# Performance work log

Hardware: AMD Instinct MI355X
Metric: run time of the kernel (lower is better)

## Reference

```python
import jax, jax.numpy as jnp
from jax import lax
import numpy as np

B, T, TW, EW = 32, 64, 32, 300   # dialogues, utterances, words, word-embed
H = 512                          # lstm hidden per direction
E = 2 * H                        # utterance embedding size
HH = 512                         # emotion hidden size
C = 7                            # output classes


def setup_inputs() -> dict:
    key = jax.random.key(0)
    ks = jax.random.split(key, 24)
    n = lambda k, shp: (jax.random.normal(k, shp, dtype=jnp.float32) * 0.05)
    inp = {
        "input_data": jax.random.normal(ks[0], (B, T, TW, EW), dtype=jnp.float32),
        # BiLSTM (torch gate order i,f,g,o)
        "lstm_Wih_f": n(ks[1], (4 * H, EW)), "lstm_Whh_f": n(ks[2], (4 * H, H)), "lstm_b_f": n(ks[3], (4 * H,)),
        "lstm_Wih_b": n(ks[4], (4 * H, EW)), "lstm_Whh_b": n(ks[5], (4 * H, H)), "lstm_b_b": n(ks[6], (4 * H,)),
        # attention weight
        "W_att": n(ks[7], (E, E)),
        # global-state GRUCell (torch gate order r,z,n)
        "g_Wih": n(ks[8], (3 * E, E)), "g_Whh": n(ks[9], (3 * E, E)), "g_bih": n(ks[10], (3 * E,)), "g_bhh": n(ks[11], (3 * E,)),
        # party-state GRUCell
        "p_Wih": n(ks[12], (3 * E, E)), "p_Whh": n(ks[13], (3 * E, E)), "p_bih": n(ks[14], (3 * E,)), "p_bhh": n(ks[15], (3 * E,)),
        # emotion-state GRUCell (input E, hidden HH)
        "e_Wih": n(ks[16], (3 * HH, E)), "e_Whh": n(ks[17], (3 * HH, HH)), "e_bih": n(ks[18], (3 * HH,)), "e_bhh": n(ks[19], (3 * HH,)),
        # classifier
        "cls_W": n(ks[20], (C, HH)), "cls_b": n(ks[21], (C,)),
    }
    return inp


def _gru_cell(x, h, Wih, Whh, bih, bhh):
    gi = x @ Wih.T + bih
    gh = h @ Whh.T + bhh
    ir, iz, inn = jnp.split(gi, 3, axis=-1)
    hr, hz, hn = jnp.split(gh, 3, axis=-1)
    r = jax.nn.sigmoid(ir + hr)
    z = jax.nn.sigmoid(iz + hz)
    n = jnp.tanh(inn + r * hn)
    return (1.0 - z) * n + z * h


def _lstm_last_hidden(xs, Wih, Whh, b):
    # xs: [Tw, N, Ew] -> final hidden [N, H]
    N = xs.shape[1]
    h0 = jnp.zeros((N, H), xs.dtype)

    def step(carry, x):
        h, c = carry
        g = x @ Wih.T + h @ Whh.T + b
        i_, f_, g_, o_ = jnp.split(g, 4, axis=-1)
        c2 = jax.nn.sigmoid(f_) * c + jax.nn.sigmoid(i_) * jnp.tanh(g_)
        h2 = jax.nn.sigmoid(o_) * jnp.tanh(c2)
        return (h2, c2), None

    (h, _), _ = lax.scan(step, (h0, h0), xs)
    return h


def _forward(input_data, lstm_Wih_f, lstm_Whh_f, lstm_b_f, lstm_Wih_b, lstm_Whh_b, lstm_b_b,
             W_att, g_Wih, g_Whh, g_bih, g_bhh, p_Wih, p_Whh, p_bih, p_bhh,
             e_Wih, e_Whh, e_bih, e_bhh, cls_W, cls_b):
    # ---- FeatureExtraction: BiLSTM over words, take fwd-last + bwd-first hidden ----
    x = input_data.reshape(B * T, TW, EW).transpose(1, 0, 2)          # [Tw, N, Ew]
    h_fwd = _lstm_last_hidden(x, lstm_Wih_f, lstm_Whh_f, lstm_b_f)     # [N, H]
    h_bwd = _lstm_last_hidden(x[::-1], lstm_Wih_b, lstm_Whh_b, lstm_b_b)  # [N, H]
    feats = jnp.concatenate([h_fwd, h_bwd], axis=-1).reshape(B, T, E)  # [B, T, 2H]

    # ---- EmotionDetection: sequential recurrence over utterances ----
    utt = feats.transpose(1, 0, 2)                                     # [T, B, E]
    hist0 = jnp.zeros((T + 1, B, E), feats.dtype)   # global_state history (idx 0 = zero init)
    party0 = jnp.zeros((2, B, E), feats.dtype)
    emo0 = jnp.zeros((B, HH), feats.dtype)
    l_idx = jnp.arange(T + 1)[:, None]              # [T+1, 1]

    def step(carry, inp):
        hist, party, emo = carry
        x_i, i = inp
        p = i % 2
        g_prev = hist[i]                                               # global_state[i]
        new_g = _gru_cell(x_i + party[p], g_prev, g_Wih, g_Whh, g_bih, g_bhh)
        hist = hist.at[i + 1].set(new_g)
        # attention over history indices 0..i (excludes the just-appended state)
        q = x_i @ W_att                                                # [B, E]
        scores = jnp.einsum('be,lbe->lb', q, hist)                     # [T+1, B]
        scores = jnp.where(l_idx <= i, scores, -jnp.inf)
        w = jax.nn.softmax(scores, axis=0)[:, :, None]                 # [T+1, B, 1]
        context = jnp.sum(hist * w, axis=0)                            # [B, E]
        new_p = _gru_cell(x_i + context, party[p], p_Wih, p_Whh, p_bih, p_bhh)
        party = party.at[p].set(new_p)
        emo = _gru_cell(new_p, emo, e_Wih, e_Whh, e_bih, e_bhh)        # [B, HH]
        return (hist, party, emo), emo

    _, emo_seq = lax.scan(step, (hist0, party0, emo0), (utt, jnp.arange(T)))
    emo_seq = emo_seq.transpose(1, 0, 2)                               # [B, T, HH]
    return emo_seq @ cls_W.T + cls_b                                   # [B, T, C]


def reference(input_data, lstm_Wih_f, lstm_Whh_f, lstm_b_f, lstm_Wih_b, lstm_Whh_b, lstm_b_b,
              W_att, g_Wih, g_Whh, g_bih, g_bhh, p_Wih, p_Whh, p_bih, p_bhh,
              e_Wih, e_Whh, e_bih, e_bhh, cls_W, cls_b):
    return _forward(input_data, lstm_Wih_f, lstm_Whh_f, lstm_b_f, lstm_Wih_b, lstm_Whh_b, lstm_b_b,
                    W_att, g_Wih, g_Whh, g_bih, g_bhh, p_Wih, p_Whh, p_bih, p_bhh,
                    e_Wih, e_Whh, e_bih, e_bhh, cls_W, cls_b)
```

## Files before the change

kernel.cpp:

```cpp
#include <hip/hip_runtime.h>
#include <math.h>

#define B_  32
#define T_  64
#define TW_ 32
#define EW_ 300
#define H_  512
#define E_  1024
#define HH_ 512
#define C_  7
#define N_  2048

typedef float f32x4 __attribute__((ext_vector_type(4)));
typedef short s16x8 __attribute__((ext_vector_type(8)));
typedef unsigned short u16;
typedef unsigned int u32;

__device__ __forceinline__ float sigm(float x){ return 1.f/(1.f+expf(-x)); }
__device__ __forceinline__ float bf2f(u16 u){
  union{float f; unsigned v;} x; x.v = ((unsigned)u)<<16; return x.f;
}
__device__ __forceinline__ u16 f2bf(float f){
  union{float f; unsigned v;} x; x.f = f;
  unsigned r = x.v + 0x7FFF + ((x.v>>16)&1);
  return (u16)(r>>16);
}
__device__ __forceinline__ void g2lds16(const void* g, void* l){
  __builtin_amdgcn_global_load_lds((const __attribute__((address_space(1))) u32*)g,
                                   (__attribute__((address_space(3))) u32*)l, 16, 0, 0);
}

__global__ __launch_bounds__(256) void k_pack_w(
    const float* __restrict__ Wih_f, const float* __restrict__ Whh_f,
    const float* __restrict__ Wih_b, const float* __restrict__ Whh_b,
    u16* __restrict__ Wpk)
{
  size_t idx = (size_t)blockIdx.x*256 + threadIdx.x;
  if(idx >= (size_t)32*26*4096) return;
  int c   = (int)(idx & 31);
  int row = (int)((idx >> 5) & 127);
  int kc  = (int)((idx >> 12) % 26);
  int pan = (int)(idx / ((size_t)26*4096));
  int dir = pan >> 4, mt = pan & 15;
  int g = row >> 5, ml = row & 31;
  int R = g*512 + mt*32 + ml;
  int k = kc*32 + c;
  const float* Wih = dir ? Wih_b : Wih_f;
  const float* Whh = dir ? Whh_b : Whh_f;
  float v = (k < 320) ? ((k < EW_) ? Wih[(size_t)R*EW_ + k] : 0.f)
                      : Whh[(size_t)R*H_ + (k-320)];
  Wpk[idx] = f2bf(v);
}

__global__ __launch_bounds__(256) void k_pack_x(
    const float* __restrict__ input, u16* __restrict__ xpk)
{
  size_t idx = (size_t)blockIdx.x*256 + threadIdx.x;
  if(idx >= (size_t)32*16*10*4096) return;
  int c   = (int)(idx & 31);
  int row = (int)((idx >> 5) & 127);
  int kc  = (int)((idx >> 12) % 10);
  int q2  = (int)((idx >> 12) / 10);
  int nt  = q2 & 15, wt = q2 >> 4;
  int n = nt*128 + row;
  int k = kc*32 + c;
  float v = (k < EW_) ? input[((size_t)n*TW_ + wt)*EW_ + k] : 0.f;
  xpk[idx] = f2bf(v);
}

__global__ __launch_bounds__(256) void k_f2bf(const float* __restrict__ src,
                                              u16* __restrict__ dst, int n)
{
  int idx = blockIdx.x*256 + threadIdx.x;
  if(idx < n) dst[idx] = f2bf(src[idx]);
}

__global__ __launch_bounds__(256) void k_wattT(const float* __restrict__ W,
                                               u16* __restrict__ dst)
{
  int idx = blockIdx.x*256 + threadIdx.x;
  if(idx >= E_*E_) return;
  int j = idx >> 10, k = idx & 1023;
  dst[idx] = f2bf(W[(size_t)k*E_ + j]);
}

__global__ __launch_bounds__(256) void lstm3(
    const u16* __restrict__ xpk, const u16* __restrict__ Wpk,
    const float* __restrict__ b_f, const float* __restrict__ b_b,
    const u16* __restrict__ hpk_in, u16* __restrict__ hpk_out,
    float* __restrict__ cb, u16* __restrict__ featsbf, int t)
{
  const int panel = blockIdx.x, nt = blockIdx.y;
  const int dir = panel & 1, mt = panel >> 1;
  const int wt = dir ? (TW_-1-t) : t;
  const u16* srcW = Wpk + (size_t)(dir*16+mt)*26*4096;
  const u16* srcX = xpk + (size_t)(wt*16+nt)*10*4096;
  const u16* srcH = hpk_in + (size_t)(dir*16+nt)*16*4096;

  __shared__ __align__(16) u16 As[3][4096];
  __shared__ __align__(16) u16 Bs[3][4096];

  const int tid = threadIdx.x;
  const int w = tid >> 6, l = tid & 63;
  const int lr = l & 15, lh = l >> 4;
  const int wn = w >> 1, wm = w & 1;

  f32x4 acc[4][4];
  #pragma unroll
  for(int a=0;a<4;a++)
    #pragma unroll
    for(int g=0;g<4;g++) acc[a][g] = (f32x4){0.f,0.f,0.f,0.f};

  auto stage = [&](int kc, int b){
    const u16* aB = (kc < 10) ? (srcX + (size_t)kc*4096) : (srcH + (size_t)(kc-10)*4096);
    const u16* bB = srcW + (size_t)kc*4096;
    #pragma unroll
    for(int c=0;c<2;++c){
      const int cc = w*2 + c;
      g2lds16((const char*)aB + cc*1024 + l*16, (char*)&As[b][0] + cc*1024);
      g2lds16((const char*)bB + cc*1024 + l*16, (char*)&Bs[b][0] + cc*1024);
    }
  };

  stage(0, 0);
  stage(1, 1);
  #pragma unroll
  for(int kc=0; kc<26; ++kc){
    if(kc < 25) asm volatile("s_waitcnt vmcnt(4)" ::: "memory");
    else        asm volatile("s_waitcnt vmcnt(0)" ::: "memory");
    __builtin_amdgcn_s_barrier();
    __builtin_amdgcn_sched_barrier(0);
    if(kc+2 < 26) stage(kc+2, (kc+2)%3);
    const int cu = kc % 3;
    s16x8 av[4], bv[4];
    #pragma unroll
    for(int nf=0; nf<4; ++nf)
      av[nf] = *(const s16x8*)&As[cu][(wn*64 + nf*16 + lr)*32 + lh*8];
    #pragma unroll
    for(int g=0; g<4; ++g)
      bv[g] = *(const s16x8*)&Bs[cu][(g*32 + wm*16 + lr)*32 + lh*8];
    #pragma unroll
    for(int g=0; g<4; ++g)
      #pragma unroll
      for(int nf=0; nf<4; ++nf)
        acc[nf][g] = __builtin_amdgcn_mfma_f32_16x16x32_bf16(av[nf], bv[g], acc[nf][g], 0,0,0);
  }

  const float* bias = dir ? b_b : b_f;
  const int col = wm*16 + lr;
  const int m = mt*32 + col;
  const float bi = bias[m], bfv = bias[H_+m], bg = bias[2*H_+m], bo = bias[3*H_+m];
  float* cbp = cb + (size_t)dir*N_*H_;
  u16* hop = hpk_out + ((size_t)(dir*16+nt)*16 + mt)*4096;
  const int n0 = nt*128;
  #pragma unroll
  for(int nf=0; nf<4; ++nf){
    #pragma unroll
    for(int r=0; r<4; ++r){
      const int row = wn*64 + nf*16 + lh*4 + r;
      const int n = n0 + row;
      float gi = acc[nf][0][r] + bi;
      float gf = acc[nf][1][r] + bfv;
      float gc = acc[nf][2][r] + bg;
      float go = acc[nf][3][r] + bo;
      float c_old = cbp[(size_t)n*H_ + m];
      float c2 = sigm(gf)*c_old + sigm(gi)*tanhf(gc);
      float h2 = sigm(go)*tanhf(c2);
      cbp[(size_t)n*H_ + m] = c2;
      if(t == TW_-1) featsbf[(size_t)n*E_ + dir*H_ + m] = f2bf(h2);
      else           hop[row*32 + col] = f2bf(h2);
    }
  }
}

__global__ __launch_bounds__(256) void k_qgemm(const u16* __restrict__ featsbf,
                                               const u16* __restrict__ WattT,
                                               float* __restrict__ q)
{
  const int n0 = blockIdx.x*64, j0 = blockIdx.y*64;
  __shared__ __align__(16) u16 As[64*40];
  __shared__ __align__(16) u16 Bs[64*40];
  const int tid = threadIdx.x;
  const int w = tid>>6, l = tid&63, lr = l&15, lk = (l>>4)*8;
  const int arow = tid>>2, ak8 = (tid&3)*8;

  f32x4 acc[4];
  #pragma unroll
  for(int i=0;i<4;i++) acc[i] = (f32x4){0.f,0.f,0.f,0.f};

  for(int kc=0; kc<32; ++kc){
    *(s16x8*)&As[arow*40 + ak8] = *(const s16x8*)&featsbf[(size_t)(n0+arow)*E_ + kc*32 + ak8];
    *(s16x8*)&Bs[arow*40 + ak8] = *(const s16x8*)&WattT[(size_t)(j0+arow)*E_ + kc*32 + ak8];
    __syncthreads();
    s16x8 av = *(const s16x8*)&As[(w*16 + lr)*40 + lk];
    #pragma unroll
    for(int mf=0; mf<4; ++mf){
      s16x8 bv = *(const s16x8*)&Bs[(mf*16 + lr)*40 + lk];
      acc[mf] = __builtin_amdgcn_mfma_f32_16x16x32_bf16(av, bv, acc[mf], 0,0,0);
    }
    __syncthreads();
  }
  #pragma unroll
  for(int mf=0; mf<4; ++mf)
    #pragma unroll
    for(int r=0; r<4; ++r){
      int n = n0 + w*16 + (l>>4)*4 + r;
      q[(size_t)n*E_ + j0 + mf*16 + lr] = acc[mf][r];
    }
}

struct GArg2 {
  const u16* xA; const u16* xB;
  long ldA; long ldB;
  const u16* W; int K;
};

__device__ __forceinline__ void gemm32v2(const GArg2 a, int R, int xt, int ks,
                                         int KS, int z, float* __restrict__ part,
                                         char* smem)
{
  u16* Xs0 = (u16*)smem;
  u16* Xs1 = Xs0 + 32*40;
  u16* Ws0 = Xs1 + 32*40;
  u16* Ws1 = Ws0 + 128*32;
  const int Kc = a.K / KS;
  const int nch = Kc >> 5;
  const int kb0 = ks * Kc;
  const int tid = threadIdx.x;
  const int w = tid>>6, l = tid&63, lr = l&15, lh = l>>4;

  f32x4 a00={0,0,0,0}, a01={0,0,0,0}, a10={0,0,0,0}, a11={0,0,0,0};

  auto issueW = [&](int c, u16* Wb){
    const int kb = kb0 + c*32;
    #pragma unroll
    for(int c2=0;c2<2;++c2){
      const int cc = w*2 + c2;
      const char* g = (const char*)(a.W + (size_t)(xt*128 + cc*16 + (l>>2))*a.K + kb) + (l&3)*16;
      g2lds16(g, (char*)Wb + cc*1024);
    }
  };
  auto loadX = [&](int c, short4* xr){
    const int kb = kb0 + c*32;
    const int row = tid>>3, k4 = (tid&7)*4;
    short4 xv = *(const short4*)&a.xA[(size_t)row*a.ldA + kb + k4];
    if(a.xB){
      short4 yv = *(const short4*)&a.xB[(size_t)row*a.ldB + kb + k4];
      xv.x = (short)f2bf(bf2f((u16)xv.x)+bf2f((u16)yv.x));
      xv.y = (short)f2bf(bf2f((u16)xv.y)+bf2f((u16)yv.y));
      xv.z = (short)f2bf(bf2f((u16)xv.z)+bf2f((u16)yv.z));
      xv.w = (short)f2bf(bf2f((u16)xv.w)+bf2f((u16)yv.w));
    }
    *xr = xv;
  };
  auto writeX = [&](short4 xv, u16* Xb){
    *(short4*)&Xb[(tid>>3)*40 + (tid&7)*4] = xv;
  };

  short4 xr;
  issueW(0, Ws0); loadX(0, &xr); writeX(xr, Xs0);
  __syncthreads();
  for(int c=0;c<nch;++c){
    u16* Xc = (c&1)?Xs1:Xs0; u16* Wc = (c&1)?Ws1:Ws0;
    u16* Xn = (c&1)?Xs0:Xs1; u16* Wn = (c&1)?Ws0:Ws1;
    const bool pre = (c+1 < nch);
    if(pre){ issueW(c+1, Wn); loadX(c+1, &xr); }
    s16x8 av0 = *(const s16x8*)&Xc[lr*40 + lh*8];
    s16x8 av1 = *(const s16x8*)&Xc[(16+lr)*40 + lh*8];
    s16x8 bv0 = *(const s16x8*)&Wc[(w*32 + lr)*32 + lh*8];
    s16x8 bv1 = *(const s16x8*)&Wc[(w*32 + 16 + lr)*32 + lh*8];
    a00 = __builtin_amdgcn_mfma_f32_16x16x32_bf16(av0, bv0, a00, 0,0,0);
    a01 = __builtin_amdgcn_mfma_f32_16x16x32_bf16(av0, bv1, a01, 0,0,0);
    a10 = __builtin_amdgcn_mfma_f32_16x16x32_bf16(av1, bv0, a10, 0,0,0);
    a11 = __builtin_amdgcn_mfma_f32_16x16x32_bf16(av1, bv1, a11, 0,0,0);
    if(pre) writeX(xr, Xn);
    __syncthreads();
  }
  float* dst = part + (size_t)((z*KS + ks)*B_)*R + xt*128 + w*32;
  f32x4 accs[2][2] = {{a00,a01},{a10,a11}};
  #pragma unroll
  for(int nf=0; nf<2; ++nf)
    #pragma unroll
    for(int mf=0; mf<2; ++mf)
      #pragma unroll
      for(int r=0; r<4; ++r){
        int n = nf*16 + lh*4 + r;
        dst[(size_t)n*R + mf*16 + lr] = accs[nf][mf][r];
      }
}

__device__ __forceinline__ void att_body(const float* __restrict__ q,
                                         const u16* __restrict__ histbf,
                                         const u16* __restrict__ featsbf,
                                         u16* __restrict__ xcbf,
                                         int i, int b, char* smem)
{
  float* qs = (float*)smem;
  float* sc = qs + E_;
  const int tid = threadIdx.x;
  *(float4*)&qs[tid*4] = *(const float4*)&q[((size_t)b*T_ + i)*E_ + tid*4];
  __syncthreads();
  const int wv = tid>>6, ln = tid&63;
  for(int L = wv; L <= i; L += 4){
    const u16* hl = histbf + ((size_t)L*B_ + b)*E_;
    float s = 0.f;
    s16x8 h0 = *(const s16x8*)&hl[ln*16];
    s16x8 h1 = *(const s16x8*)&hl[ln*16 + 8];
    #pragma unroll
    for(int j=0;j<8;j++){
      s += qs[ln*16 + j]     * bf2f((u16)h0[j]);
      s += qs[ln*16 + 8 + j] * bf2f((u16)h1[j]);
    }
    #pragma unroll
    for(int off=32; off; off>>=1) s += __shfl_down(s, off);
    if(ln == 0) sc[L] = s;
  }
  __syncthreads();
  if(tid < 64){
    float v  = (tid <= i) ? sc[tid] : -INFINITY;
    float mx = v;
    #pragma unroll
    for(int off=32; off; off>>=1) mx = fmaxf(mx, __shfl_xor(mx, off));
    float ex = (tid <= i) ? expf(v - mx) : 0.f;
    float sm = ex;
    #pragma unroll
    for(int off=32; off; off>>=1) sm += __shfl_xor(sm, off);
    sc[tid] = ex / sm;
  }
  __syncthreads();
  const int e4 = tid*4;
  float c0=0.f, c1=0.f, c2=0.f, c3=0.f;
  for(int L=0; L<=i; ++L){
    float wl = sc[L];
    short4 hv = *(const short4*)&histbf[((size_t)L*B_ + b)*E_ + e4];
    c0 += wl*bf2f((u16)hv.x);
    c1 += wl*bf2f((u16)hv.y);
    c2 += wl*bf2f((u16)hv.z);
    c3 += wl*bf2f((u16)hv.w);
  }
  const u16* xi = featsbf + ((size_t)b*T_ + i)*E_ + e4;
  xcbf[(size_t)b*E_ + e4 + 0] = f2bf(bf2f(xi[0]) + c0);
  xcbf[(size_t)b*E_ + e4 + 1] = f2bf(bf2f(xi[1]) + c1);
  xcbf[(size_t)b*E_ + e4 + 2] = f2bf(bf2f(xi[2]) + c2);
  xcbf[(size_t)b*E_ + e4 + 3] = f2bf(bf2f(xi[3]) + c3);
}

__device__ __forceinline__ void gru_comb(const float* __restrict__ part, int R, int J, int KS,
                                         const float* __restrict__ bih, const float* __restrict__ bhh,
                                         const float* __restrict__ hprev_f,
                                         float* __restrict__ dst_f,
                                         u16* __restrict__ dstbf,
                                         float* __restrict__ dst_seq, int idx)
{
  const int b = idx / J, e = idx - b*J;
  float ir=0.f, iz=0.f, in_=0.f, hr=0.f, hz=0.f, hn=0.f;
  for(int ks=0; ks<KS; ++ks){
    const float* p0 = part + (size_t)(ks*B_ + b)*R;
    const float* p1 = part + (size_t)((KS+ks)*B_ + b)*R;
    ir += p0[e]; iz += p0[J+e]; in_ += p0[2*J+e];
    hr += p1[e]; hz += p1[J+e]; hn  += p1[2*J+e];
  }
  ir += bih[e]; iz += bih[J+e]; in_ += bih[2*J+e];
  hr += bhh[e]; hz += bhh[J+e]; hn  += bhh[2*J+e];
  const float r = sigm(ir + hr);
  const float z = sigm(iz + hz);
  const float n = tanhf(in_ + r*hn);
  const float hp = hprev_f[(size_t)b*J + e];
  const float h2 = (1.f - z)*n + z*hp;
  dst_f[(size_t)b*J + e] = h2;
  dstbf[(size_t)b*J + e] = f2bf(h2);
  if(dst_seq) dst_seq[(size_t)b*J + e] = h2;
}

__global__ __launch_bounds__(256) void k_A(GArg2 g0, GArg2 g1, GArg2 e0, GArg2 e1,
    float* __restrict__ part_g, float* __restrict__ part_e,
    const float* __restrict__ q, const u16* __restrict__ histbf,
    const u16* __restrict__ featsbf, u16* __restrict__ xcbf, int i)
{
  __shared__ __align__(16) char smem[21504];
  const int x = blockIdx.x;
  if(x < 384){
    if(i >= T_) return;
    const int xt = x % 24, ks = (x/24) & 7, z = x/192;
    gemm32v2(z ? g1 : g0, 3*E_, xt, ks, 8, z, part_g, smem);
  } else if(x < 576){
    if(i < 1) return;
    const int ix = x-384, xt = ix % 12, ks = (ix/12) & 7, z = ix/96;
    gemm32v2(z ? e1 : e0, 3*HH_, xt, ks, 8, z, part_e, smem);
  } else {
    if(i >= T_) return;
    att_body(q, histbf, featsbf, xcbf, i, x-576, smem);
  }
}

__global__ __launch_bounds__(256) void k_B(GArg2 p0, GArg2 p1,
    const float* __restrict__ part_g, const float* __restrict__ part_e,
    const float* __restrict__ g_bih, const float* __restrict__ g_bhh,
    const float* __restrict__ e_bih, const float* __restrict__ e_bhh,
    const float* __restrict__ gf_prev, float* __restrict__ gf_next,
    u16* __restrict__ histbf,
    float* __restrict__ emof, u16* __restrict__ emobf,
    float* __restrict__ emo_seq, float* __restrict__ part_p, int i)
{
  __shared__ __align__(16) char smem[21504];
  const int x = blockIdx.x;
  if(x < 128){
    if(i >= T_) return;
    gru_comb(part_g, 3*E_, E_, 8, g_bih, g_bhh,
             gf_prev, gf_next, histbf + (size_t)(i+1)*B_*E_, nullptr,
             x*256 + (int)threadIdx.x);
  } else if(x < 512){
    if(i >= T_) return;
    const int ix = x-128, xt = ix % 24, ks = (ix/24) & 7, z = ix/192;
    gemm32v2(z ? p1 : p0, 3*E_, xt, ks, 8, z, part_p, smem);
  } else {
    if(i < 1) return;
    gru_comb(part_e, 3*HH_, HH_, 8, e_bih, e_bhh,
             emof, emof, emobf, emo_seq + (size_t)(i-1)*B_*HH_,
             (x-512)*256 + (int)threadIdx.x);
  }
}

__global__ __launch_bounds__(256) void k_C(const float* __restrict__ part_p,
    const float* __restrict__ p_bih, const float* __restrict__ p_bhh,
    float* __restrict__ partyf_p, u16* __restrict__ partybf_p)
{
  const int idx = blockIdx.x*256 + threadIdx.x;
  gru_comb(part_p, 3*E_, E_, 8, p_bih, p_bhh, partyf_p, partyf_p, partybf_p, nullptr, idx);
}

__global__ __launch_bounds__(256) void classify(const float* __restrict__ emo_seq,
    const float* __restrict__ clsW, const float* __restrict__ clsb, float* __restrict__ out)
{
  const int idx = blockIdx.x*256 + threadIdx.x;
  if(idx >= B_*T_*C_) return;
  const int c = idx % C_;
  const int bt = idx / C_;
  const int t = bt % T_, b = bt / T_;
  const float* e = emo_seq + (size_t)(t*B_ + b)*HH_;
  const float* w = clsW + (size_t)c*HH_;
  float s = clsb[c];
  for(int h=0; h<HH_; ++h) s += e[h]*w[h];
  out[idx] = s;
}

extern "C" void kernel_launch(void* const* d_in, const int* in_sizes, int n_in,
                              void* d_out, int out_size, void* d_ws, size_t ws_size,
                              hipStream_t stream)
{
  const float* input  = (const float*)d_in[0];
  const float* Wih_f  = (const float*)d_in[1];
  const float* Whh_f  = (const float*)d_in[2];
  const float* b_f    = (const float*)d_in[3];
  const float* Wih_b  = (const float*)d_in[4];
  const float* Whh_b  = (const float*)d_in[5];
  const float* b_b    = (const float*)d_in[6];
  const float* W_att  = (const float*)d_in[7];
  const float* g_Wih  = (const float*)d_in[8];
  const float* g_Whh  = (const float*)d_in[9];
  const float* g_bih  = (const float*)d_in[10];
  const float* g_bhh  = (const float*)d_in[11];
  const float* p_Wih  = (const float*)d_in[12];
  const float* p_Whh  = (const float*)d_in[13];
  const float* p_bih  = (const float*)d_in[14];
  const float* p_bhh  = (const float*)d_in[15];
  const float* e_Wih  = (const float*)d_in[16];
  const float* e_Whh  = (const float*)d_in[17];
  const float* e_bih  = (const float*)d_in[18];
  const float* e_bhh  = (const float*)d_in[19];
  const float* cls_W  = (const float*)d_in[20];
  const float* cls_b  = (const float*)d_in[21];

  char* base = (char*)d_ws;
  size_t off = 0;
  auto alloc = [&](size_t bytes)->char*{
    char* p = base + off; off += (bytes + 255) & ~(size_t)255; return p;
  };
  u16*   Wpk     = (u16*)alloc((size_t)32*26*4096*2);
  u16*   xpk     = (u16*)alloc((size_t)32*16*10*4096*2);
  u16*   hpkA    = (u16*)alloc((size_t)2*16*16*4096*2);
  u16*   hpkB    = (u16*)alloc((size_t)2*16*16*4096*2);
  float* cb      = (float*)alloc((size_t)2*N_*H_*4);
  u16*   featsbf = (u16*)alloc((size_t)N_*E_*2);
  u16*   eWih    = (u16*)alloc((size_t)3*HH_*E_*2);
  u16*   eWhh    = (u16*)alloc((size_t)3*HH_*HH_*2);
  u16*   histbf  = (u16*)alloc((size_t)(T_+1)*B_*E_*2);
  float* gfbuf   = (float*)alloc((size_t)2*B_*E_*4);
  float* partyf  = (float*)alloc((size_t)2*B_*E_*4);
  u16*   partybf = (u16*)alloc((size_t)2*B_*E_*2);
  float* emof    = (float*)alloc((size_t)B_*HH_*4);
  u16*   emobf   = (u16*)alloc((size_t)B_*HH_*2);
  float* emo_seq = (float*)alloc((size_t)T_*B_*HH_*4);
  u16*   xcbf    = (u16*)alloc((size_t)B_*E_*2);
  u16*   gWih    = (u16*)((char*)xpk + 0);
  u16*   gWhh    = (u16*)((char*)xpk + 6291456);
  u16*   pWih    = (u16*)((char*)xpk + 12582912);
  u16*   pWhh    = (u16*)((char*)xpk + 18874368);
  float* part_e  = (float*)((char*)xpk + 25165824);
  float* q       = (float*)((char*)xpk + 28311552);
  u16*   WattT   = (u16*)((char*)xpk + 36700160);
  float* part_g  = (float*)cb;
  float* part_p  = (float*)hpkA;

  hipMemsetAsync(hpkA,    0, (size_t)2*16*16*4096*2, stream);
  hipMemsetAsync(cb,      0, (size_t)2*N_*H_*4, stream);
  hipMemsetAsync(histbf,  0, (size_t)B_*E_*2, stream);
  hipMemsetAsync(gfbuf,   0, (size_t)B_*E_*4, stream);
  hipMemsetAsync(partyf,  0, (size_t)2*B_*E_*4, stream);
  hipMemsetAsync(partybf, 0, (size_t)2*B_*E_*2, stream);
  hipMemsetAsync(emof,    0, (size_t)B_*HH_*4, stream);
  hipMemsetAsync(emobf,   0, (size_t)B_*HH_*2, stream);

  k_pack_w<<<dim3(((size_t)32*26*4096 + 255)/256), 256, 0, stream>>>(Wih_f, Whh_f, Wih_b, Whh_b, Wpk);
  k_pack_x<<<dim3(((size_t)32*16*10*4096 + 255)/256), 256, 0, stream>>>(input, xpk);

  for(int t=0; t<TW_; ++t){
    u16* hin  = (t & 1) ? hpkB : hpkA;
    u16* hout = (t & 1) ? hpkA : hpkB;
    lstm3<<<dim3(32, 16), 256, 0, stream>>>(xpk, Wpk, b_f, b_b, hin, hout, cb, featsbf, t);
  }

  k_f2bf<<<dim3((3*E_*E_+255)/256), 256, 0, stream>>>(g_Wih, gWih, 3*E_*E_);
  k_f2bf<<<dim3((3*E_*E_+255)/256), 256, 0, stream>>>(g_Whh, gWhh, 3*E_*E_);
  k_f2bf<<<dim3((3*E_*E_+255)/256), 256, 0, stream>>>(p_Wih, pWih, 3*E_*E_);
  k_f2bf<<<dim3((3*E_*E_+255)/256), 256, 0, stream>>>(p_Whh, pWhh, 3*E_*E_);
  k_f2bf<<<dim3((3*HH_*E_+255)/256), 256, 0, stream>>>(e_Wih, eWih, 3*HH_*E_);
  k_f2bf<<<dim3((3*HH_*HH_+255)/256), 256, 0, stream>>>(e_Whh, eWhh, 3*HH_*HH_);
  k_wattT<<<dim3((E_*E_+255)/256), 256, 0, stream>>>(W_att, WattT);

  k_qgemm<<<dim3(32, 16), 256, 0, stream>>>(featsbf, WattT, q);

  for(int i=0; i<=T_; ++i){
    const int p  = i & 1;
    const int pe = (i-1) & 1;
    GArg2 ga0{ featsbf + (size_t)i*E_, partybf + (size_t)p*B_*E_, (long)T_*E_, (long)E_, gWih, E_ };
    GArg2 ga1{ histbf + (size_t)i*B_*E_, nullptr, (long)E_, 0, gWhh, E_ };
    GArg2 ea0{ partybf + (size_t)pe*B_*E_, nullptr, (long)E_, 0, eWih, E_ };
    GArg2 ea1{ emobf, nullptr, (long)HH_, 0, eWhh, HH_ };
    k_A<<<dim3(608), 256, 0, stream>>>(ga0, ga1, ea0, ea1, part_g, part_e,
                                       q, histbf, featsbf, xcbf, i);
    GArg2 pa0{ xcbf, nullptr, (long)E_, 0, pWih, E_ };
    GArg2 pa1{ partybf + (size_t)p*B_*E_, nullptr, (long)E_, 0, pWhh, E_ };
    k_B<<<dim3(576), 256, 0, stream>>>(pa0, pa1, part_g, part_e,
                                       g_bih, g_bhh, e_bih, e_bhh,
                                       gfbuf + (size_t)(i&1)*B_*E_,
                                       gfbuf + (size_t)((i+1)&1)*B_*E_,
                                       histbf, emof, emobf, emo_seq, part_p, i);
    if(i < T_){
      k_C<<<dim3(128), 256, 0, stream>>>(part_p, p_bih, p_bhh,
                                         partyf + (size_t)p*B_*E_,
                                         partybf + (size_t)p*B_*E_);
    }
  }

  classify<<<dim3((B_*T_*C_+255)/256), 256, 0, stream>>>(emo_seq, cls_W, cls_b, (float*)d_out);
}
```

Before: 2.666 ms.

## Fuse word-LSTM timesteps into one persistent kernel with group barriers

Replaces the 32 per-timestep LSTM launches with a single persistent kernel of 512 blocks that loops over time. The cell state now stays in registers instead of a global buffer, and each timestep synchronizes on per-group atomic counters, where a group is the 16 blocks sharing a direction and batch tile. The x-projection tiles for the next step are prefetched before the spin-wait. This removes launch overhead and the global cell-state traffic, but it requires all 512 blocks to be co-resident. With launch_bounds(256,2) that holds only if the device has enough CUs, otherwise the spin barrier can deadlock.

```diff
diff --git a/kernel.cpp b/kernel.cpp
--- a/kernel.cpp
+++ b/kernel.cpp
@@ -84,18 +84,16 @@
   dst[idx] = f2bf(W[(size_t)k*E_ + j]);
 }
 
-__global__ __launch_bounds__(256) void lstm3(
+__global__ __launch_bounds__(256, 2) void lstm_p(
     const u16* __restrict__ xpk, const u16* __restrict__ Wpk,
     const float* __restrict__ b_f, const float* __restrict__ b_b,
-    const u16* __restrict__ hpk_in, u16* __restrict__ hpk_out,
-    float* __restrict__ cb, u16* __restrict__ featsbf, int t)
-{
-  const int panel = blockIdx.x, nt = blockIdx.y;
-  const int dir = panel & 1, mt = panel >> 1;
-  const int wt = dir ? (TW_-1-t) : t;
+    u16* __restrict__ hpkA, u16* __restrict__ hpkB,
+    u16* __restrict__ featsbf, u32* __restrict__ bar)
+{
+  const int bx = blockIdx.x;
+  const int g  = bx & 31, mt = bx >> 5;
+  const int dir = g & 1, nt = g >> 1;
   const u16* srcW = Wpk + (size_t)(dir*16+mt)*26*4096;
-  const u16* srcX = xpk + (size_t)(wt*16+nt)*10*4096;
-  const u16* srcH = hpk_in + (size_t)(dir*16+nt)*16*4096;
 
   __shared__ __align__(16) u16 As[3][4096];
   __shared__ __align__(16) u16 Bs[3][4096];
@@ -105,14 +103,17 @@
   const int lr = l & 15, lh = l >> 4;
   const int wn = w >> 1, wm = w & 1;
 
-  f32x4 acc[4][4];
+  const float* bias = dir ? b_b : b_f;
+  const int col = wm*16 + lr;
+  const int m = mt*32 + col;
+  const float bi = bias[m], bfv = bias[H_+m], bg = bias[2*H_+m], bo = bias[3*H_+m];
+
+  float creg[4][4];
   #pragma unroll
-  for(int a=0;a<4;a++)
-    #pragma unroll
-    for(int g=0;g<4;g++) acc[a][g] = (f32x4){0.f,0.f,0.f,0.f};
-
-  auto stage = [&](int kc, int b){
-    const u16* aB = (kc < 10) ? (srcX + (size_t)kc*4096) : (srcH + (size_t)(kc-10)*4096);
+  for(int a=0;a<4;a++){ creg[a][0]=0.f; creg[a][1]=0.f; creg[a][2]=0.f; creg[a][3]=0.f; }
+
+  auto stage = [&](const u16* sX, const u16* sH, int kc, int b){
+    const u16* aB = (kc < 10) ? (sX + (size_t)kc*4096) : (sH + (size_t)(kc-10)*4096);
     const u16* bB = srcW + (size_t)kc*4096;
     #pragma unroll
     for(int c=0;c<2;++c){
@@ -122,53 +123,85 @@
     }
   };
 
-  stage(0, 0);
-  stage(1, 1);
-  #pragma unroll
-  for(int kc=0; kc<26; ++kc){
-    if(kc < 25) asm volatile("s_waitcnt vmcnt(4)" ::: "memory");
-    else        asm volatile("s_waitcnt vmcnt(0)" ::: "memory");
-    __builtin_amdgcn_s_barrier();
-    __builtin_amdgcn_sched_barrier(0);
-    if(kc+2 < 26) stage(kc+2, (kc+2)%3);
-    const int cu = kc % 3;
-    s16x8 av[4], bv[4];
-    #pragma unroll
-    for(int nf=0; nf<4; ++nf)
-      av[nf] = *(const s16x8*)&As[cu][(wn*64 + nf*16 + lr)*32 + lh*8];
-    #pragma unroll
-    for(int g=0; g<4; ++g)
-      bv[g] = *(const s16x8*)&Bs[cu][(g*32 + wm*16 + lr)*32 + lh*8];
-    #pragma unroll
-    for(int g=0; g<4; ++g)
+  {
+    const int wt0 = dir ? (TW_-1) : 0;
+    const u16* sX0 = xpk + (size_t)(wt0*16+nt)*10*4096;
+    stage(sX0, nullptr, 0, 0);
+    stage(sX0, nullptr, 1, 1);
+  }
+
+  #pragma unroll 1
+  for(int t=0; t<TW_; ++t){
+    const int wt = dir ? (TW_-1-t) : t;
+    const u16* sX = xpk + (size_t)(wt*16+nt)*10*4096;
+    const u16* hin  = (t & 1) ? hpkB : hpkA;
+    u16*       hout = (t & 1) ? hpkA : hpkB;
+    const u16* sH = hin + (size_t)(dir*16+nt)*16*4096;
+
+    f32x4 acc[4][4];
+    #pragma unroll
+    for(int a=0;a<4;a++)
+      #pragma unroll
+      for(int gg=0;gg<4;gg++) acc[a][gg] = (f32x4){0.f,0.f,0.f,0.f};
+
+    #pragma unroll
+    for(int kc=0; kc<26; ++kc){
+      if(kc < 25) asm volatile("s_waitcnt vmcnt(4)" ::: "memory");
+      else        asm volatile("s_waitcnt vmcnt(0)" ::: "memory");
+      __builtin_amdgcn_s_barrier();
+      __builtin_amdgcn_sched_barrier(0);
+      if(kc+2 < 26) stage(sX, sH, kc+2, (kc+2)%3);
+      const int cu = kc % 3;
+      s16x8 av[4], bv[4];
       #pragma unroll
       for(int nf=0; nf<4; ++nf)
-        acc[nf][g] = __builtin_amdgcn_mfma_f32_16x16x32_bf16(av[nf], bv[g], acc[nf][g], 0,0,0);
-  }
-
-  const float* bias = dir ? b_b : b_f;
-  const int col = wm*16 + lr;
-  const int m = mt*32 + col;
-  const float bi = bias[m], bfv = bias[H_+m], bg = bias[2*H_+m], bo = bias[3*H_+m];
-  float* cbp = cb + (size_t)dir*N_*H_;
-  u16* hop = hpk_out + ((size_t)(dir*16+nt)*16 + mt)*4096;
-  const int n0 = nt*128;
-  #pragma unroll
-  for(int nf=0; nf<4; ++nf){
-    #pragma unroll
-    for(int r=0; r<4; ++r){
-      const int row = wn*64 + nf*16 + lh*4 + r;
-      const int n = n0 + row;
-      float gi = acc[nf][0][r] + bi;
-      float gf = acc[nf][1][r] + bfv;
-      float gc = acc[nf][2][r] + bg;
-      float go = acc[nf][3][r] + bo;
-      float c_old = cbp[(size_t)n*H_ + m];
-      float c2 = sigm(gf)*c_old + sigm(gi)*tanhf(gc);
-      float h2 = sigm(go)*tanhf(c2);
-      cbp[(size_t)n*H_ + m] = c2;
-      if(t == TW_-1) featsbf[(size_t)n*E_ + dir*H_ + m] = f2bf(h2);
-      else           hop[row*32 + col] = f2bf(h2);
+        av[nf] = *(const s16x8*)&As[cu][(wn*64 + nf*16 + lr)*32 + lh*8];
+      #pragma unroll
+      for(int gg=0; gg<4; ++gg)
+        bv[gg] = *(const s16x8*)&Bs[cu][(gg*32 + wm*16 + lr)*32 + lh*8];
+      #pragma unroll
+      for(int gg=0; gg<4; ++gg)
+        #pragma unroll
+        for(int nf=0; nf<4; ++nf)
+          acc[nf][gg] = __builtin_amdgcn_mfma_f32_16x16x32_bf16(av[nf], bv[gg], acc[nf][gg], 0,0,0);
+    }
+    __builtin_amdgcn_s_barrier();
+
+    u16* hop = hout + ((size_t)(dir*16+nt)*16 + mt)*4096;
+    const int n0 = nt*128;
+    #pragma unroll
+    for(int nf=0; nf<4; ++nf){
+      #pragma unroll
+      for(int r=0; r<4; ++r){
+        const int row = wn*64 + nf*16 + lh*4 + r;
+        float gi = acc[nf][0][r] + bi;
+        float gf = acc[nf][1][r] + bfv;
+        float gc = acc[nf][2][r] + bg;
+        float go = acc[nf][3][r] + bo;
+        float c2 = sigm(gf)*creg[nf][r] + sigm(gi)*tanhf(gc);
+        float h2 = sigm(go)*tanhf(c2);
+        creg[nf][r] = c2;
+        if(t == TW_-1) featsbf[(size_t)(n0+row)*E_ + dir*H_ + m] = f2bf(h2);
+        else           hop[row*32 + col] = f2bf(h2);
+      }
+    }
+
+    if(t < TW_-1){
+      __threadfence();
+      if(tid == 0)
+        __hip_atomic_fetch_add(&bar[g], 1u, __ATOMIC_RELEASE, __HIP_MEMORY_SCOPE_AGENT);
+      {
+        const int wt2 = dir ? (TW_-1-(t+1)) : (t+1);
+        const u16* sX2 = xpk + (size_t)(wt2*16+nt)*10*4096;
+        stage(sX2, nullptr, 0, 0);
+        stage(sX2, nullptr, 1, 1);
+      }
+      if(tid == 0){
+        const u32 want = (u32)(16*(t+1));
+        while(__hip_atomic_load(&bar[g], __ATOMIC_ACQUIRE, __HIP_MEMORY_SCOPE_AGENT) < want)
+          __builtin_amdgcn_s_sleep(2);
+      }
+      __syncthreads();
     }
   }
 }
@@ -480,7 +513,6 @@
   u16*   xpk     = (u16*)alloc((size_t)32*16*10*4096*2);
   u16*   hpkA    = (u16*)alloc((size_t)2*16*16*4096*2);
   u16*   hpkB    = (u16*)alloc((size_t)2*16*16*4096*2);
-  float* cb      = (float*)alloc((size_t)2*N_*H_*4);
   u16*   featsbf = (u16*)alloc((size_t)N_*E_*2);
   u16*   eWih    = (u16*)alloc((size_t)3*HH_*E_*2);
   u16*   eWhh    = (u16*)alloc((size_t)3*HH_*HH_*2);
@@ -492,6 +524,8 @@
   u16*   emobf   = (u16*)alloc((size_t)B_*HH_*2);
   float* emo_seq = (float*)alloc((size_t)T_*B_*HH_*4);
   u16*   xcbf    = (u16*)alloc((size_t)B_*E_*2);
+  float* part_p  = (float*)alloc((size_t)16*B_*3*E_*4);
+  u32*   bar     = (u32*)alloc(32*sizeof(u32));
   u16*   gWih    = (u16*)((char*)xpk + 0);
   u16*   gWhh    = (u16*)((char*)xpk + 6291456);
   u16*   pWih    = (u16*)((char*)xpk + 12582912);
@@ -499,11 +533,10 @@
   float* part_e  = (float*)((char*)xpk + 25165824);
   float* q       = (float*)((char*)xpk + 28311552);
   u16*   WattT   = (u16*)((char*)xpk + 36700160);
-  float* part_g  = (float*)cb;
-  float* part_p  = (float*)hpkA;
+  float* part_g  = (float*)hpkA;
 
   hipMemsetAsync(hpkA,    0, (size_t)2*16*16*4096*2, stream);
-  hipMemsetAsync(cb,      0, (size_t)2*N_*H_*4, stream);
+  hipMemsetAsync(bar,     0, 32*sizeof(u32), stream);
   hipMemsetAsync(histbf,  0, (size_t)B_*E_*2, stream);
   hipMemsetAsync(gfbuf,   0, (size_t)B_*E_*4, stream);
   hipMemsetAsync(partyf,  0, (size_t)2*B_*E_*4, stream);
@@ -514,11 +547,7 @@
   k_pack_w<<<dim3(((size_t)32*26*4096 + 255)/256), 256, 0, stream>>>(Wih_f, Whh_f, Wih_b, Whh_b, Wpk);
   k_pack_x<<<dim3(((size_t)32*16*10*4096 + 255)/256), 256, 0, stream>>>(input, xpk);
 
-  for(int t=0; t<TW_; ++t){
-    u16* hin  = (t & 1) ? hpkB : hpkA;
-    u16* hout = (t & 1) ? hpkA : hpkB;
-    lstm3<<<dim3(32, 16), 256, 0, stream>>>(xpk, Wpk, b_f, b_b, hin, hout, cb, featsbf, t);
-  }
+  lstm_p<<<dim3(512), 256, 0, stream>>>(xpk, Wpk, b_f, b_b, hpkA, hpkB, featsbf, bar);
 
   k_f2bf<<<dim3((3*E_*E_+255)/256), 256, 0, stream>>>(g_Wih, gWih, 3*E_*E_);
   k_f2bf<<<dim3((3*E_*E_+255)/256), 256, 0, stream>>>(g_Whh, gWhh, 3*E_*E_);
```

Measured after the change: 4.640 ms. 1.74x slower.
